# Kernel optimization log

Hardware: AMD Instinct MI355X
Metric: run time of the kernel (lower is better)

## Reference

```python
import jax, jax.numpy as jnp
import numpy as np

FILTERS = 128

def setup_inputs() -> dict:
    key = jax.random.key(0)
    ks = jax.random.split(key, 8)
    B, Nq, Nkv, C = 4, 4096, 4096, 128
    q_inputs = jax.random.normal(ks[0], (B, Nq, C), dtype=jnp.float32)
    kv_inputs = jax.random.normal(ks[1], (B, Nkv, C), dtype=jnp.float32)
    s = 1.0 / np.sqrt(C)
    Wq = jax.random.normal(ks[2], (C, FILTERS), dtype=jnp.float32) * s
    Wk = jax.random.normal(ks[3], (C, FILTERS), dtype=jnp.float32) * s
    Wv = jax.random.normal(ks[4], (C, FILTERS), dtype=jnp.float32) * s
    bq = jnp.zeros((FILTERS,), jnp.float32)
    bk = jnp.zeros((FILTERS,), jnp.float32)
    bv = jnp.zeros((FILTERS,), jnp.float32)
    return {"q_inputs": q_inputs, "kv_inputs": kv_inputs,
            "Wq": Wq, "bq": bq, "Wk": Wk, "bk": bk, "Wv": Wv, "bv": bv}

def reference(q_inputs, kv_inputs, Wq, bq, Wk, bk, Wv, bv):
    # Dense projections (last-axis matmul + bias)
    q = jnp.einsum('bnc,cf->bnf', q_inputs, Wq) + bq
    k = jnp.einsum('bmc,cf->bmf', kv_inputs, Wk) + bk
    v = jnp.einsum('bmc,cf->bmf', kv_inputs, Wv) + bv
    scale = jnp.sqrt(jnp.asarray(FILTERS, jnp.float32))
    scores = jnp.einsum('bnf,bmf->bnm', q, k) / scale  # [B, Nq, Nkv]
    weights = jax.nn.softmax(scores, axis=-1)
    return jnp.einsum('bnm,bmf->bnf', weights, v)
```

## Files before the change

kernel.cpp:

```cpp
#include <hip/hip_runtime.h>
#include <stdint.h>

typedef unsigned short u16;
typedef __bf16 bf16x8 __attribute__((ext_vector_type(8)));
typedef unsigned short u16x8 __attribute__((ext_vector_type(8)));
typedef unsigned short u16x4 __attribute__((ext_vector_type(4)));
typedef float f32x4 __attribute__((ext_vector_type(4)));

#define MFMA16(a, b, c) __builtin_amdgcn_mfma_f32_16x16x32_bf16((a), (b), (c), 0, 0, 0)

__device__ __forceinline__ u16 f2b(float f) {
    union { unsigned int i; float f; } v; v.f = f;
    unsigned int r = (v.i + 0x7FFFu + ((v.i >> 16) & 1u)) >> 16;
    return (u16)r;
}

constexpr int N = 4096;
constexpr int Cc = 128;
constexpr int Fc = 128;
constexpr int BATCH = 4;

constexpr int XS_STRIDE = 136;
constexpr int WT_STRIDE = 136;
constexpr int KS_STRIDE = 136;
constexpr int VTS_STRIDE = 136;
constexpr int PS_STRIDE = 40;
constexpr int OM_STRIDE = 132;

__global__ __launch_bounds__(256) void wtrans_kernel(
    const float* __restrict__ Wq, const float* __restrict__ Wk,
    const float* __restrict__ Wv, u16* __restrict__ WtG)
{
    __shared__ __align__(16) u16 Wl[128 * 132];
    const int tid = threadIdx.x;
    const int which = blockIdx.x;
    const float* W = which == 0 ? Wq : (which == 1 ? Wk : Wv);
#pragma unroll
    for (int it = 0; it < 16; ++it) {
        int idx4 = tid + it * 256; int e0 = idx4 * 4;
        int c = e0 >> 7, f = e0 & 127;
        float4 wv = *(const float4*)(W + e0);
        u16x4 h; h[0] = f2b(wv.x); h[1] = f2b(wv.y); h[2] = f2b(wv.z); h[3] = f2b(wv.w);
        *(u16x4*)&Wl[c * 132 + f] = h;
    }
    __syncthreads();
    u16* out = WtG + which * 16384;
#pragma unroll
    for (int it = 0; it < 8; ++it) {
        int idx8 = tid + it * 256; int e0 = idx8 * 8;
        int f = e0 >> 7, c = e0 & 127;
        u16x8 h;
#pragma unroll
        for (int j = 0; j < 8; ++j) h[j] = Wl[(c + j) * 132 + f];
        *(u16x8*)(out + e0) = h;
    }
}

__global__ __launch_bounds__(256) void proj_kernel(
    const float* __restrict__ q_in, const float* __restrict__ kv_in,
    const u16* __restrict__ WtG,
    const float* __restrict__ bq, const float* __restrict__ bk,
    const float* __restrict__ bv,
    u16* __restrict__ Qw, u16* __restrict__ Kw, u16* __restrict__ Vtw)
{
    __shared__ __align__(16) u16 Xs[64 * XS_STRIDE];
    __shared__ __align__(16) u16 Wt[128 * WT_STRIDE];

    const int tid = threadIdx.x;
    const int which = blockIdx.y;
    const int b = blockIdx.z;
    const int m0 = blockIdx.x * 64;

    const float* X = (which == 0 ? q_in : kv_in) + ((size_t)b * N + m0) * Cc;
    const u16* Wsrc = WtG + which * 16384;
    const float* bias = which == 0 ? bq : (which == 1 ? bk : bv);

#pragma unroll
    for (int it = 0; it < 8; ++it) {
        int idx4 = tid + it * 256; int e0 = idx4 * 4;
        int r = e0 >> 7, c = e0 & 127;
        float4 xv = *(const float4*)(X + e0);
        u16x4 h; h[0] = f2b(xv.x); h[1] = f2b(xv.y); h[2] = f2b(xv.z); h[3] = f2b(xv.w);
        *(u16x4*)&Xs[r * XS_STRIDE + c] = h;
    }
#pragma unroll
    for (int it = 0; it < 8; ++it) {
        int idx8 = tid + it * 256; int e0 = idx8 * 8;
        int f = e0 >> 7, c = e0 & 127;
        *(u16x8*)&Wt[f * WT_STRIDE + c] = *(const u16x8*)(Wsrc + e0);
    }
    __syncthreads();

    const int lane = tid & 63;
    const int w = tid >> 6;
    const int n16 = lane & 15;
    const int quad = lane >> 4;

    if (which < 2) {
        bf16x8 ax[4];
#pragma unroll
        for (int kk = 0; kk < 4; ++kk)
            ax[kk] = *(const bf16x8*)&Xs[(w * 16 + n16) * XS_STRIDE + kk * 32 + quad * 8];
        const float scale = (which == 0) ? 0.08838834764831845f : 1.0f;
        u16* Out = (which == 0) ? Qw : Kw;
#pragma unroll
        for (int ft = 0; ft < 8; ++ft) {
            f32x4 acc = {0.f, 0.f, 0.f, 0.f};
#pragma unroll
            for (int kk = 0; kk < 4; ++kk) {
                bf16x8 bw = *(const bf16x8*)&Wt[(ft * 16 + n16) * WT_STRIDE + kk * 32 + quad * 8];
                acc = MFMA16(ax[kk], bw, acc);
            }
            float bias_f = bias[ft * 16 + n16];
#pragma unroll
            for (int r = 0; r < 4; ++r) {
                int row = m0 + w * 16 + quad * 4 + r;
                Out[((size_t)b * N + row) * Fc + ft * 16 + n16] = f2b((acc[r] + bias_f) * scale);
            }
        }
    } else {
#pragma unroll
        for (int ft2 = 0; ft2 < 2; ++ft2) {
            int ftg = w * 2 + ft2;
            bf16x8 aw[4];
#pragma unroll
            for (int kk = 0; kk < 4; ++kk)
                aw[kk] = *(const bf16x8*)&Wt[(ftg * 16 + n16) * WT_STRIDE + kk * 32 + quad * 8];
            float bias4[4];
#pragma unroll
            for (int r = 0; r < 4; ++r) bias4[r] = bias[ftg * 16 + quad * 4 + r];
#pragma unroll
            for (int nt = 0; nt < 4; ++nt) {
                f32x4 acc = {0.f, 0.f, 0.f, 0.f};
#pragma unroll
                for (int kk = 0; kk < 4; ++kk) {
                    bf16x8 bx = *(const bf16x8*)&Xs[(nt * 16 + n16) * XS_STRIDE + kk * 32 + quad * 8];
                    acc = MFMA16(aw[kk], bx, acc);
                }
#pragma unroll
                for (int r = 0; r < 4; ++r) {
                    int fg = ftg * 16 + quad * 4 + r;
                    int rowg = m0 + nt * 16 + n16;
                    Vtw[((size_t)b * Fc + fg) * N + rowg] = f2b(acc[r] + bias4[r]);
                }
            }
        }
    }
}

__global__ __launch_bounds__(512, 2) void attn_kernel(
    const u16* __restrict__ Qw, const u16* __restrict__ Kw,
    const u16* __restrict__ Vtw, float* __restrict__ out)
{
    __shared__ __align__(16) char smem_raw[102400];
    u16* Ks  = (u16*)smem_raw;
    u16* Vts = Ks + 128 * KS_STRIDE;
    u16* Ps  = Vts + 128 * VTS_STRIDE;
    float* Om = (float*)smem_raw;
    float* Lm = Om + 6 * 32 * OM_STRIDE;

    const int tid = threadIdx.x;
    const int b = blockIdx.y;
    const int q0 = blockIdx.x * 64;
    const int lane = tid & 63;
    const int w = tid >> 6;
    const int kg = w & 3;
    const int qg = w >> 2;
    const int n16 = lane & 15;
    const int quad = lane >> 4;

    bf16x8 aq[2][4];
#pragma unroll
    for (int qs = 0; qs < 2; ++qs) {
        const u16* qrow = Qw + ((size_t)b * N + q0 + qg * 32 + qs * 16 + n16) * Cc;
#pragma unroll
        for (int kk = 0; kk < 4; ++kk)
            aq[qs][kk] = *(const bf16x8*)(qrow + kk * 32 + quad * 8);
    }

    int rr[4], cc[4];
#pragma unroll
    for (int it = 0; it < 4; ++it) {
        int idx8 = tid + it * 512; int e0 = idx8 * 8;
        rr[it] = e0 >> 7; cc[it] = e0 & 127;
    }
    const u16* Kbase = Kw + (size_t)b * N * Cc;
    const u16* Vbase = Vtw + (size_t)b * Fc * N;

    u16x8 kreg[4], vreg[4];
#pragma unroll
    for (int it = 0; it < 4; ++it) {
        kreg[it] = *(const u16x8*)(Kbase + (size_t)rr[it] * Cc + cc[it]);
        vreg[it] = *(const u16x8*)(Vbase + (size_t)rr[it] * N + cc[it]);
    }

    f32x4 o[2][8];
#pragma unroll
    for (int qs = 0; qs < 2; ++qs)
#pragma unroll
        for (int ct = 0; ct < 8; ++ct) o[qs][ct] = (f32x4){0.f, 0.f, 0.f, 0.f};
    float lloc[2] = {0.f, 0.f};

    u16* Psw = Ps + w * 32 * PS_STRIDE;

    for (int t = 0; t < N / 128; ++t) {
#pragma unroll
        for (int it = 0; it < 4; ++it) {
            *(u16x8*)&Ks[rr[it] * KS_STRIDE + cc[it]] = kreg[it];
            *(u16x8*)&Vts[rr[it] * VTS_STRIDE + cc[it]] = vreg[it];
        }
        __syncthreads();

        if (t + 1 < N / 128) {
            int k0n = (t + 1) * 128;
#pragma unroll
            for (int it = 0; it < 4; ++it) {
                kreg[it] = *(const u16x8*)(Kbase + (size_t)(k0n + rr[it]) * Cc + cc[it]);
                vreg[it] = *(const u16x8*)(Vbase + (size_t)rr[it] * N + k0n + cc[it]);
            }
        }

        bf16x8 ak[2][4];
#pragma unroll
        for (int ks = 0; ks < 2; ++ks)
#pragma unroll
            for (int kk = 0; kk < 4; ++kk)
                ak[ks][kk] = *(const bf16x8*)&Ks[(kg * 32 + ks * 16 + n16) * KS_STRIDE + kk * 32 + quad * 8];

        f32x4 st[2][2];
#pragma unroll
        for (int qs = 0; qs < 2; ++qs)
#pragma unroll
            for (int ks = 0; ks < 2; ++ks) {
                f32x4 acc = {0.f, 0.f, 0.f, 0.f};
#pragma unroll
                for (int kk = 0; kk < 4; ++kk)
                    acc = MFMA16(ak[ks][kk], aq[qs][kk], acc);
                st[qs][ks] = acc;
            }

#pragma unroll
        for (int qs = 0; qs < 2; ++qs)
#pragma unroll
            for (int ks = 0; ks < 2; ++ks) {
                float e0 = __expf(st[qs][ks][0]), e1 = __expf(st[qs][ks][1]);
                float e2 = __expf(st[qs][ks][2]), e3 = __expf(st[qs][ks][3]);
                lloc[qs] += (e0 + e1) + (e2 + e3);
                u16x4 pk; pk[0] = f2b(e0); pk[1] = f2b(e1); pk[2] = f2b(e2); pk[3] = f2b(e3);
                *(u16x4*)&Psw[(qs * 16 + n16) * PS_STRIDE + ks * 16 + quad * 4] = pk;
            }

        bf16x8 pa[2];
#pragma unroll
        for (int qs = 0; qs < 2; ++qs)
            pa[qs] = *(const bf16x8*)&Psw[(qs * 16 + n16) * PS_STRIDE + quad * 8];
#pragma unroll
        for (int ct = 0; ct < 8; ++ct) {
            bf16x8 bv_ = *(const bf16x8*)&Vts[(ct * 16 + n16) * VTS_STRIDE + kg * 32 + quad * 8];
            o[0][ct] = MFMA16(pa[0], bv_, o[0][ct]);
            o[1][ct] = MFMA16(pa[1], bv_, o[1][ct]);
        }
        __syncthreads();
    }

    float lv[2];
#pragma unroll
    for (int qs = 0; qs < 2; ++qs) {
        float v = lloc[qs];
        v += __shfl_xor(v, 16);
        v += __shfl_xor(v, 32);
        lv[qs] = v;
    }

    if (kg != 0) {
#pragma unroll
        for (int qs = 0; qs < 2; ++qs) {
#pragma unroll
            for (int ct = 0; ct < 8; ++ct)
#pragma unroll
                for (int r = 0; r < 4; ++r)
                    Om[((size_t)((kg - 1) * 2 + qg) * 32 + qs * 16 + quad * 4 + r) * OM_STRIDE + ct * 16 + n16] = o[qs][ct][r];
            if (quad == 0) Lm[(kg - 1) * 64 + qg * 32 + qs * 16 + n16] = lv[qs];
        }
    }
    __syncthreads();
    if (kg == 0) {
#pragma unroll
        for (int qs = 0; qs < 2; ++qs) {
            float lsum[4];
#pragma unroll
            for (int r = 0; r < 4; ++r) {
                float s = __shfl(lv[qs], quad * 4 + r);
#pragma unroll
                for (int j = 0; j < 3; ++j)
                    s += Lm[j * 64 + qg * 32 + qs * 16 + quad * 4 + r];
                lsum[r] = s;
            }
#pragma unroll
            for (int ct = 0; ct < 8; ++ct) {
#pragma unroll
                for (int r = 0; r < 4; ++r) {
                    float ov = o[qs][ct][r];
#pragma unroll
                    for (int j = 0; j < 3; ++j)
                        ov += Om[((size_t)(j * 2 + qg) * 32 + qs * 16 + quad * 4 + r) * OM_STRIDE + ct * 16 + n16];
                    int q = q0 + qg * 32 + qs * 16 + quad * 4 + r;
                    out[((size_t)b * N + q) * Fc + ct * 16 + n16] = ov / lsum[r];
                }
            }
        }
    }
}

extern "C" void kernel_launch(void* const* d_in, const int* in_sizes, int n_in,
                              void* d_out, int out_size, void* d_ws, size_t ws_size,
                              hipStream_t stream) {
    (void)in_sizes; (void)n_in; (void)out_size; (void)ws_size;
    const float* q_in  = (const float*)d_in[0];
    const float* kv_in = (const float*)d_in[1];
    const float* Wq = (const float*)d_in[2];
    const float* bq = (const float*)d_in[3];
    const float* Wk = (const float*)d_in[4];
    const float* bk = (const float*)d_in[5];
    const float* Wv = (const float*)d_in[6];
    const float* bv = (const float*)d_in[7];

    const size_t qkv = (size_t)BATCH * N * Fc;
    u16* Qw  = (u16*)d_ws;
    u16* Kw  = Qw + qkv;
    u16* Vtw = Kw + qkv;
    u16* WtG = Vtw + qkv;

    wtrans_kernel<<<dim3(3), dim3(256), 0, stream>>>(Wq, Wk, Wv, WtG);
    proj_kernel<<<dim3(64, 3, BATCH), dim3(256), 0, stream>>>(
        q_in, kv_in, WtG, bq, bk, bv, Qw, Kw, Vtw);
    attn_kernel<<<dim3(64, BATCH), dim3(512), 0, stream>>>(
        Qw, Kw, Vtw, (float*)d_out);
}
```

Measured before the change: 139.4 us.

## Rework attention kernel with 32x32 MFMA, async LDS loads, XOR swizzle, double buffering

The attention kernel now uses 32x32x16 MFMA tiles, so each wave holds Q for 32 rows. Softmax probabilities are rearranged in registers with permlane32_swap instead of going through LDS. K and V tiles are loaded straight into double-buffered LDS with global_load_lds, and the projection kernel writes K and V pre-swizzled (XOR) so the unpadded LDS reads avoid bank conflicts. Blocks are remapped across batches, and the final reduction is done by all threads with vectorized stores. LDS use rises to about 134KB per block, which may limit occupancy to one block per CU despite launch_bounds(512,2).

```diff
diff --git a/kernel.cpp b/kernel.cpp
--- a/kernel.cpp
+++ b/kernel.cpp
@@ -2,30 +2,39 @@
 #include <stdint.h>
 
 typedef unsigned short u16;
+typedef unsigned int u32;
 typedef __bf16 bf16x8 __attribute__((ext_vector_type(8)));
 typedef unsigned short u16x8 __attribute__((ext_vector_type(8)));
 typedef unsigned short u16x4 __attribute__((ext_vector_type(4)));
 typedef float f32x4 __attribute__((ext_vector_type(4)));
+typedef float f32x16 __attribute__((ext_vector_type(16)));
 
 #define MFMA16(a, b, c) __builtin_amdgcn_mfma_f32_16x16x32_bf16((a), (b), (c), 0, 0, 0)
+#define MFMA32(a, b, c) __builtin_amdgcn_mfma_f32_32x32x16_bf16((a), (b), (c), 0, 0, 0)
 
 __device__ __forceinline__ u16 f2b(float f) {
     union { unsigned int i; float f; } v; v.f = f;
     unsigned int r = (v.i + 0x7FFFu + ((v.i >> 16) & 1u)) >> 16;
     return (u16)r;
 }
+__device__ __forceinline__ u32 pk2(float lo, float hi) {
+    return (u32)f2b(lo) | ((u32)f2b(hi) << 16);
+}
+__device__ __forceinline__ void gload16(const void* g, void* l) {
+    __builtin_amdgcn_global_load_lds(
+        (const __attribute__((address_space(1))) u32*)g,
+        (__attribute__((address_space(3))) u32*)l, 16, 0, 0);
+}
 
 constexpr int N = 4096;
 constexpr int Cc = 128;
 constexpr int Fc = 128;
 constexpr int BATCH = 4;
+constexpr int NT = N / 128;
 
 constexpr int XS_STRIDE = 136;
 constexpr int WT_STRIDE = 136;
-constexpr int KS_STRIDE = 136;
-constexpr int VTS_STRIDE = 136;
-constexpr int PS_STRIDE = 40;
-constexpr int OM_STRIDE = 132;
+constexpr int OM_STRIDE = 130;
 
 __global__ __launch_bounds__(256) void wtrans_kernel(
     const float* __restrict__ Wq, const float* __restrict__ Wk,
@@ -102,6 +111,7 @@
         for (int kk = 0; kk < 4; ++kk)
             ax[kk] = *(const bf16x8*)&Xs[(w * 16 + n16) * XS_STRIDE + kk * 32 + quad * 8];
         const float scale = (which == 0) ? 0.08838834764831845f : 1.0f;
+        const int swmask = (which == 1) ? 7 : 0;
         u16* Out = (which == 0) ? Qw : Kw;
 #pragma unroll
         for (int ft = 0; ft < 8; ++ft) {
@@ -115,7 +125,9 @@
 #pragma unroll
             for (int r = 0; r < 4; ++r) {
                 int row = m0 + w * 16 + quad * 4 + r;
-                Out[((size_t)b * N + row) * Fc + ft * 16 + n16] = f2b((acc[r] + bias_f) * scale);
+                int f = ft * 16 + n16;
+                int fs = f ^ ((row & swmask) << 3);
+                Out[((size_t)b * N + row) * Fc + fs] = f2b((acc[r] + bias_f) * scale);
             }
         }
     } else {
@@ -141,7 +153,8 @@
                 for (int r = 0; r < 4; ++r) {
                     int fg = ftg * 16 + quad * 4 + r;
                     int rowg = m0 + nt * 16 + n16;
-                    Vtw[((size_t)b * Fc + fg) * N + rowg] = f2b(acc[r] + bias4[r]);
+                    int rs = rowg ^ ((fg & 7) << 3);
+                    Vtw[((size_t)b * Fc + fg) * N + rs] = f2b(acc[r] + bias4[r]);
                 }
             }
         }
@@ -152,163 +165,157 @@
     const u16* __restrict__ Qw, const u16* __restrict__ Kw,
     const u16* __restrict__ Vtw, float* __restrict__ out)
 {
-    __shared__ __align__(16) char smem_raw[102400];
-    u16* Ks  = (u16*)smem_raw;
-    u16* Vts = Ks + 128 * KS_STRIDE;
-    u16* Ps  = Vts + 128 * VTS_STRIDE;
-    float* Om = (float*)smem_raw;
-    float* Lm = Om + 6 * 32 * OM_STRIDE;
+    __shared__ __align__(16) char smem[134144];
+    u16* const Ks0 = (u16*)smem;
+    u16* const Ks1 = (u16*)(smem + 32768);
+    u16* const Vs0 = (u16*)(smem + 65536);
+    u16* const Vs1 = (u16*)(smem + 98304);
 
     const int tid = threadIdx.x;
-    const int b = blockIdx.y;
-    const int q0 = blockIdx.x * 64;
+    const int id = blockIdx.x + 64 * blockIdx.y;
+    const int b = (id >> 1) & 3;
+    const int q0 = (((id & 1) << 5) + (id >> 3)) << 6;
+
     const int lane = tid & 63;
     const int w = tid >> 6;
     const int kg = w & 3;
     const int qg = w >> 2;
-    const int n16 = lane & 15;
-    const int quad = lane >> 4;
-
-    bf16x8 aq[2][4];
-#pragma unroll
-    for (int qs = 0; qs < 2; ++qs) {
-        const u16* qrow = Qw + ((size_t)b * N + q0 + qg * 32 + qs * 16 + n16) * Cc;
-#pragma unroll
-        for (int kk = 0; kk < 4; ++kk)
-            aq[qs][kk] = *(const bf16x8*)(qrow + kk * 32 + quad * 8);
-    }
-
-    int rr[4], cc[4];
-#pragma unroll
-    for (int it = 0; it < 4; ++it) {
-        int idx8 = tid + it * 512; int e0 = idx8 * 8;
-        rr[it] = e0 >> 7; cc[it] = e0 & 127;
-    }
-    const u16* Kbase = Kw + (size_t)b * N * Cc;
-    const u16* Vbase = Vtw + (size_t)b * Fc * N;
-
-    u16x8 kreg[4], vreg[4];
-#pragma unroll
-    for (int it = 0; it < 4; ++it) {
-        kreg[it] = *(const u16x8*)(Kbase + (size_t)rr[it] * Cc + cc[it]);
-        vreg[it] = *(const u16x8*)(Vbase + (size_t)rr[it] * N + cc[it]);
-    }
-
-    f32x4 o[2][8];
-#pragma unroll
-    for (int qs = 0; qs < 2; ++qs)
-#pragma unroll
-        for (int ct = 0; ct < 8; ++ct) o[qs][ct] = (f32x4){0.f, 0.f, 0.f, 0.f};
-    float lloc[2] = {0.f, 0.f};
-
-    u16* Psw = Ps + w * 32 * PS_STRIDE;
-
-    for (int t = 0; t < N / 128; ++t) {
+    const int l31 = lane & 31;
+    const int hi = lane >> 5;
+
+    bf16x8 aq[8];
+    {
+        const u16* qp = Qw + ((size_t)b * N + q0 + qg * 32 + l31) * Cc + hi * 8;
+#pragma unroll
+        for (int kk = 0; kk < 8; ++kk) aq[kk] = *(const bf16x8*)(qp + kk * 16);
+    }
+
+    const u16* const Kb = Kw + (size_t)b * N * Cc;
+    const u16* const Vb = Vtw + (size_t)b * Fc * N;
+
+    const int rk = kg * 32 + l31;
+    const int swk = (rk & 7) << 3;
+    int koff[8];
+#pragma unroll
+    for (int kk = 0; kk < 8; ++kk)
+        koff[kk] = rk * 128 + (((kk * 2 + hi) * 8) ^ swk);
+    int voff[4][2];
+#pragma unroll
+    for (int cb = 0; cb < 4; ++cb) {
+        int rv = cb * 32 + l31;
+        int swv = (rv & 7) << 3;
+#pragma unroll
+        for (int ks = 0; ks < 2; ++ks)
+            voff[cb][ks] = rv * 128 + (((kg * 4 + ks * 2 + hi) * 8) ^ swv);
+    }
+
+    f32x16 o[4];
+#pragma unroll
+    for (int cb = 0; cb < 4; ++cb)
+#pragma unroll
+        for (int i = 0; i < 16; ++i) o[cb][i] = 0.f;
+    float lloc = 0.f;
+
+    int ci[4];
+#pragma unroll
+    for (int it = 0; it < 4; ++it) ci[it] = tid + it * 512;
+
+    auto STAGE = [&](u16* kd, u16* vd, int t) {
+        const u16* ksrc = Kb + (size_t)t * (128 * 128);
+        const u16* vsrc = Vb + t * 128;
 #pragma unroll
         for (int it = 0; it < 4; ++it) {
-            *(u16x8*)&Ks[rr[it] * KS_STRIDE + cc[it]] = kreg[it];
-            *(u16x8*)&Vts[rr[it] * VTS_STRIDE + cc[it]] = vreg[it];
-        }
+            gload16(ksrc + ci[it] * 8, kd + ci[it] * 8);
+            gload16(vsrc + (size_t)(ci[it] >> 4) * N + (ci[it] & 15) * 8, vd + ci[it] * 8);
+        }
+    };
+
+    auto TILE_STEP = [&](const u16* Ksb, const u16* Vsb) {
+        f32x16 st;
+#pragma unroll
+        for (int i = 0; i < 16; ++i) st[i] = 0.f;
+#pragma unroll
+        for (int kk = 0; kk < 8; ++kk) {
+            bf16x8 ak = *(const bf16x8*)(Ksb + koff[kk]);
+            st = MFMA32(ak, aq[kk], st);
+        }
+        float p[16];
+#pragma unroll
+        for (int i = 0; i < 16; ++i) p[i] = __expf(st[i]);
+        lloc += ((((p[0] + p[1]) + (p[2] + p[3])) + ((p[4] + p[5]) + (p[6] + p[7])))
+               + (((p[8] + p[9]) + (p[10] + p[11])) + ((p[12] + p[13]) + (p[14] + p[15]))));
+        bf16x8 pb[2];
+#pragma unroll
+        for (int ks = 0; ks < 2; ++ks) {
+            u32 a0 = pk2(p[ks * 8 + 0], p[ks * 8 + 1]);
+            u32 a1 = pk2(p[ks * 8 + 2], p[ks * 8 + 3]);
+            u32 a2 = pk2(p[ks * 8 + 4], p[ks * 8 + 5]);
+            u32 a3 = pk2(p[ks * 8 + 6], p[ks * 8 + 7]);
+            auto s02 = __builtin_amdgcn_permlane32_swap(a0, a2, false, false);
+            auto s13 = __builtin_amdgcn_permlane32_swap(a1, a3, false, false);
+            union { u32 u[4]; bf16x8 v; } bb;
+            bb.u[0] = s02[0]; bb.u[1] = s13[0]; bb.u[2] = s02[1]; bb.u[3] = s13[1];
+            pb[ks] = bb.v;
+        }
+#pragma unroll
+        for (int cb = 0; cb < 4; ++cb) {
+#pragma unroll
+            for (int ks = 0; ks < 2; ++ks) {
+                bf16x8 av = *(const bf16x8*)(Vsb + voff[cb][ks]);
+                o[cb] = MFMA32(av, pb[ks], o[cb]);
+            }
+        }
+    };
+
+    STAGE(Ks0, Vs0, 0);
+    __syncthreads();
+    for (int t = 0; t < NT; t += 2) {
+        if (t + 1 < NT) STAGE(Ks1, Vs1, t + 1);
+        TILE_STEP(Ks0, Vs0);
         __syncthreads();
-
-        if (t + 1 < N / 128) {
-            int k0n = (t + 1) * 128;
-#pragma unroll
-            for (int it = 0; it < 4; ++it) {
-                kreg[it] = *(const u16x8*)(Kbase + (size_t)(k0n + rr[it]) * Cc + cc[it]);
-                vreg[it] = *(const u16x8*)(Vbase + (size_t)rr[it] * N + k0n + cc[it]);
-            }
-        }
-
-        bf16x8 ak[2][4];
-#pragma unroll
-        for (int ks = 0; ks < 2; ++ks)
-#pragma unroll
-            for (int kk = 0; kk < 4; ++kk)
-                ak[ks][kk] = *(const bf16x8*)&Ks[(kg * 32 + ks * 16 + n16) * KS_STRIDE + kk * 32 + quad * 8];
-
-        f32x4 st[2][2];
-#pragma unroll
-        for (int qs = 0; qs < 2; ++qs)
-#pragma unroll
-            for (int ks = 0; ks < 2; ++ks) {
-                f32x4 acc = {0.f, 0.f, 0.f, 0.f};
-#pragma unroll
-                for (int kk = 0; kk < 4; ++kk)
-                    acc = MFMA16(ak[ks][kk], aq[qs][kk], acc);
-                st[qs][ks] = acc;
-            }
-
-#pragma unroll
-        for (int qs = 0; qs < 2; ++qs)
-#pragma unroll
-            for (int ks = 0; ks < 2; ++ks) {
-                float e0 = __expf(st[qs][ks][0]), e1 = __expf(st[qs][ks][1]);
-                float e2 = __expf(st[qs][ks][2]), e3 = __expf(st[qs][ks][3]);
-                lloc[qs] += (e0 + e1) + (e2 + e3);
-                u16x4 pk; pk[0] = f2b(e0); pk[1] = f2b(e1); pk[2] = f2b(e2); pk[3] = f2b(e3);
-                *(u16x4*)&Psw[(qs * 16 + n16) * PS_STRIDE + ks * 16 + quad * 4] = pk;
-            }
-
-        bf16x8 pa[2];
-#pragma unroll
-        for (int qs = 0; qs < 2; ++qs)
-            pa[qs] = *(const bf16x8*)&Psw[(qs * 16 + n16) * PS_STRIDE + quad * 8];
-#pragma unroll
-        for (int ct = 0; ct < 8; ++ct) {
-            bf16x8 bv_ = *(const bf16x8*)&Vts[(ct * 16 + n16) * VTS_STRIDE + kg * 32 + quad * 8];
-            o[0][ct] = MFMA16(pa[0], bv_, o[0][ct]);
-            o[1][ct] = MFMA16(pa[1], bv_, o[1][ct]);
-        }
+        if (t + 2 < NT) STAGE(Ks0, Vs0, t + 2);
+        TILE_STEP(Ks1, Vs1);
         __syncthreads();
     }
 
-    float lv[2];
-#pragma unroll
-    for (int qs = 0; qs < 2; ++qs) {
-        float v = lloc[qs];
-        v += __shfl_xor(v, 16);
-        v += __shfl_xor(v, 32);
-        lv[qs] = v;
-    }
-
-    if (kg != 0) {
-#pragma unroll
-        for (int qs = 0; qs < 2; ++qs) {
-#pragma unroll
-            for (int ct = 0; ct < 8; ++ct)
-#pragma unroll
-                for (int r = 0; r < 4; ++r)
-                    Om[((size_t)((kg - 1) * 2 + qg) * 32 + qs * 16 + quad * 4 + r) * OM_STRIDE + ct * 16 + n16] = o[qs][ct][r];
-            if (quad == 0) Lm[(kg - 1) * 64 + qg * 32 + qs * 16 + n16] = lv[qs];
-        }
+    float lv = lloc + __shfl_xor(lloc, 32);
+
+    float* const Om = (float*)smem;
+    float* const Lm = (float*)(smem + 4 * 64 * OM_STRIDE * 4);
+
+    const int qrow_w = qg * 32 + l31;
+    const int crow0 = 4 * hi;
+    {
+        float* dst = Om + (size_t)(kg * 64 + qrow_w) * OM_STRIDE;
+#pragma unroll
+        for (int cb = 0; cb < 4; ++cb)
+#pragma unroll
+            for (int i = 0; i < 16; ++i) {
+                int ch = cb * 32 + (i & 3) + 8 * (i >> 2) + crow0;
+                dst[ch] = o[cb][i];
+            }
+        if (hi == 0) Lm[kg * 64 + qrow_w] = lv;
     }
     __syncthreads();
-    if (kg == 0) {
-#pragma unroll
-        for (int qs = 0; qs < 2; ++qs) {
-            float lsum[4];
-#pragma unroll
-            for (int r = 0; r < 4; ++r) {
-                float s = __shfl(lv[qs], quad * 4 + r);
-#pragma unroll
-                for (int j = 0; j < 3; ++j)
-                    s += Lm[j * 64 + qg * 32 + qs * 16 + quad * 4 + r];
-                lsum[r] = s;
-            }
-#pragma unroll
-            for (int ct = 0; ct < 8; ++ct) {
-#pragma unroll
-                for (int r = 0; r < 4; ++r) {
-                    float ov = o[qs][ct][r];
-#pragma unroll
-                    for (int j = 0; j < 3; ++j)
-                        ov += Om[((size_t)(j * 2 + qg) * 32 + qs * 16 + quad * 4 + r) * OM_STRIDE + ct * 16 + n16];
-                    int q = q0 + qg * 32 + qs * 16 + quad * 4 + r;
-                    out[((size_t)b * N + q) * Fc + ct * 16 + n16] = ov / lsum[r];
-                }
-            }
-        }
+
+    const int qrow = tid >> 3;
+    const int ch0 = (tid & 7) * 16;
+    const float lsum = Lm[qrow] + Lm[64 + qrow] + Lm[128 + qrow] + Lm[192 + qrow];
+    const float linv = 1.0f / lsum;
+    float* op = out + ((size_t)b * N + q0 + qrow) * Fc + ch0;
+#pragma unroll
+    for (int j4 = 0; j4 < 4; ++j4) {
+        f32x4 v;
+#pragma unroll
+        for (int jj = 0; jj < 4; ++jj) {
+            int ch = ch0 + j4 * 4 + jj;
+            float s = Om[(size_t)(0 * 64 + qrow) * OM_STRIDE + ch]
+                    + Om[(size_t)(1 * 64 + qrow) * OM_STRIDE + ch]
+                    + Om[(size_t)(2 * 64 + qrow) * OM_STRIDE + ch]
+                    + Om[(size_t)(3 * 64 + qrow) * OM_STRIDE + ch];
+            v[jj] = s * linv;
+        }
+        *(f32x4*)(op + j4 * 4) = v;
     }
 }
 
```

After: 133.2 us. 4.4% less time.
